# Kernel tuning notes

Measured on AMD Instinct MI355X. Metric: run time of the kernel, lower is better.

The kernel has to match this reference:

```python
import jax, jax.numpy as jnp
import numpy as np

DIM = 1024
NUM_HEADS = 16
HEAD_DIM = DIM // NUM_HEADS


def setup_inputs() -> dict:
    key = jax.random.key(0)
    k1, k2, k3, k4 = jax.random.split(key, 4)
    x = jax.random.normal(k1, (4, 4096, DIM), dtype=jnp.float32)
    # nn.Linear(dim, 3*dim, bias=False): weight [3*dim, dim]
    w_qkv = jax.random.normal(k2, (3 * DIM, DIM), dtype=jnp.float32) * (1.0 / np.sqrt(DIM))
    # nn.Linear(dim, dim): weight [dim, dim], bias [dim]
    w_proj = jax.random.normal(k3, (DIM, DIM), dtype=jnp.float32) * (1.0 / np.sqrt(DIM))
    b_proj = jax.random.normal(k4, (DIM,), dtype=jnp.float32) * 0.01
    return {"x": x, "w_qkv": w_qkv, "w_proj": w_proj, "b_proj": b_proj}


def reference(x, w_qkv, w_proj, b_proj):
    B, N, C = x.shape
    H, D = NUM_HEADS, C // NUM_HEADS
    # qkv projection: [B,N,3C] -> [3,B,H,N,D]
    qkv = (x @ w_qkv.T).reshape(B, N, 3, H, D).transpose(2, 0, 3, 1, 4)
    q, k, v = qkv[0], qkv[1], qkv[2]
    # elu(x)+1 feature map
    q = jax.nn.elu(q) + 1.0
    k = jax.nn.elu(k) + 1.0
    # kv outer-product aggregation: [B,H,D,D]
    kv = jnp.einsum('bhnd,bhne->bhde', k, v)
    # numerator: [B,H,N,D]
    num = jnp.einsum('bhnd,bhde->bhne', q, kv)
    # normalizer: [B,H,N]
    z = 1.0 / (jnp.einsum('bhnd,bhd->bhn', q, k.sum(axis=2)) + 1e-6)
    out = num * z[..., None]  # [B,H,N,D]
    out = out.transpose(0, 2, 1, 3).reshape(B, N, C)
    return out @ w_proj.T + b_proj
```

## Files before the change

kernel.cpp:

```cpp
#include <hip/hip_runtime.h>
#include <hip/hip_bf16.h>
#include <stdint.h>


typedef unsigned short u16;
typedef __attribute__((ext_vector_type(4))) float f32x4;
typedef __attribute__((ext_vector_type(8))) __bf16 bf16x8;
typedef __attribute__((ext_vector_type(4))) unsigned short us4;
typedef __attribute__((ext_vector_type(8))) unsigned short us8;

typedef __attribute__((address_space(3))) unsigned as3u;
typedef const __attribute__((address_space(1))) unsigned as1u;

__device__ __forceinline__ float bf2f(u16 u) {
  union { unsigned i; float f; } x; x.i = ((unsigned)u) << 16; return x.f;
}
__device__ __forceinline__ u16 f2bf(float f) {
  union { float f; unsigned i; } x; x.f = f;
  return (u16)((x.i + 0x7FFFu + ((x.i >> 16) & 1u)) >> 16);
}
__device__ __forceinline__ void gload16(const u16* g, u16* l) {
  __builtin_amdgcn_global_load_lds((as1u*)g, (as3u*)l, 16, 0, 0);
}
__device__ __forceinline__ bf16x8 ld8(const u16* p) { return *(const bf16x8*)p; }

#define BAR asm volatile("s_barrier" ::: "memory")
#define VMC4 asm volatile("s_waitcnt vmcnt(4)" ::: "memory")
#define VMC0 asm volatile("s_waitcnt vmcnt(0)" ::: "memory")

#define CVT_O1 4194304
#define CVT_O2 4980736
#define CVT_O3 5242880
__global__ __launch_bounds__(256) void cvt_all(
    const float* __restrict__ x, const float* __restrict__ wqkv,
    const float* __restrict__ wproj, u16* __restrict__ xb,
    u16* __restrict__ wqkvb, u16* __restrict__ wprojb) {
  int i = blockIdx.x * 256 + threadIdx.x;
  const float* src;
  u16* dst;
  int off;
  if (i < CVT_O1) { src = x; dst = xb; off = i; }
  else if (i < CVT_O2) { src = wqkv; dst = wqkvb; off = i - CVT_O1; }
  else if (i < CVT_O3) { src = wproj; dst = wprojb; off = i - CVT_O2; }
  else return;
  f32x4 v = ((const f32x4*)src)[off];
  us4 o;
  o[0] = f2bf(v[0]); o[1] = f2bf(v[1]); o[2] = f2bf(v[2]); o[3] = f2bf(v[3]);
  ((us4*)dst)[off] = o;
}

template <int EPI>
__device__ __forceinline__ void gemm256_body(
    const u16* __restrict__ A, const u16* __restrict__ B, int Ncols,
    u16* __restrict__ oQ, u16* __restrict__ oKT, u16* __restrict__ oVT,
    const float* __restrict__ bias, float* __restrict__ oF, u16* ldsb) {
  constexpr int K = 1024;
  constexpr int NITER = 8;

  const int bid = blockIdx.x;
  const int tm = (bid & 7) * 8 + ((bid >> 3) & 7);
  const int tn = bid >> 6;
  const int m0 = tm << 8, n0 = tn << 8;
  const int t = threadIdx.x;
  const int w = t >> 6, lane = t & 63;
  const int wm = w >> 2, wn = w & 3;
  const int l15 = lane & 15, l4 = lane >> 4;

  const u16* Ab = A + (size_t)m0 * K;
  const u16* Bb = B + (size_t)n0 * K;

  int srcoff[2][2];
  #pragma unroll
  for (int l = 0; l < 2; ++l) {
    int c = l * 512 + t;
    int row = c >> 3, ch = c & 7;
    #pragma unroll
    for (int h = 0; h < 2; ++h) {
      int rr = row + h * 128;
      srcoff[l][h] = rr * K + (ch ^ (rr & 7)) * 8;
    }
  }

#define LDSAT(buf, mat) (ldsb + ((buf) * 2 + (mat)) * (256 * 64))

#define STAGE(mat, buf, h, kt)                                                \
  {                                                                           \
    const u16* gsrc = ((mat) ? Bb : Ab) + (kt) * 64;                          \
    _Pragma("unroll") for (int l = 0; l < 2; ++l)                             \
        gload16(gsrc + srcoff[l][h],                                          \
                LDSAT(buf, mat) + (l * 512 + w * 64) * 8 + (h) * 128 * 64);   \
  }

#define LDA(buf, q)                                                           \
  _Pragma("unroll") for (int i = 0; i < 2; ++i)                               \
  _Pragma("unroll") for (int kk = 0; kk < 2; ++kk) {                          \
    int row = wm * 128 + (q) * 32 + i * 16 + l15;                             \
    int ch = (kk * 4 + l4) ^ (row & 7);                                       \
    a[i][kk] = ld8(LDSAT(buf, 0) + row * 64 + ch * 8);                        \
  }

#define LDB(buf)                                                              \
  _Pragma("unroll") for (int j = 0; j < 4; ++j)                               \
  _Pragma("unroll") for (int kk = 0; kk < 2; ++kk) {                          \
    int row = wn * 64 + j * 16 + l15;                                         \
    int ch = (kk * 4 + l4) ^ (row & 7);                                       \
    b[j][kk] = ld8(LDSAT(buf, 1) + row * 64 + ch * 8);                        \
  }

#define MFMA16(q)                                                             \
  __builtin_amdgcn_s_setprio(1);                                              \
  _Pragma("unroll") for (int i = 0; i < 2; ++i)                               \
  _Pragma("unroll") for (int kk = 0; kk < 2; ++kk)                            \
  _Pragma("unroll") for (int j = 0; j < 4; ++j)                               \
    acc[(q) * 2 + i][j] = __builtin_amdgcn_mfma_f32_16x16x32_bf16(            \
        a[i][kk], b[j][kk], acc[(q) * 2 + i][j], 0, 0, 0);                    \
  __builtin_amdgcn_s_setprio(0);

  f32x4 acc[8][4] = {};
  bf16x8 a[2][2], b[4][2];

  STAGE(1, 0, 0, 0); STAGE(1, 0, 1, 0);
  STAGE(0, 0, 0, 0); STAGE(0, 0, 1, 0);
  STAGE(1, 1, 0, 1); STAGE(1, 1, 1, 1);
  VMC4;
  BAR;

  for (int J = 0; J < NITER; ++J) {
    const int t2 = 2 * J + 2, t3 = 2 * J + 3;
    const bool more = (J < NITER - 1);
    LDB(0); LDA(0, 0);
    STAGE(0, 1, 0, 2 * J + 1);
    BAR; MFMA16(0); BAR;
    LDA(0, 1);
    STAGE(0, 1, 1, 2 * J + 1);
    BAR; MFMA16(1); BAR;
    LDA(0, 2);
    if (more) STAGE(1, 0, 0, t2);
    BAR; MFMA16(2); BAR;
    LDA(0, 3);
    if (more) STAGE(1, 0, 1, t2);
    BAR; MFMA16(3);
    if (more) { VMC4; } else { VMC0; }
    BAR;
    LDB(1); LDA(1, 0);
    if (more) STAGE(0, 0, 0, t2);
    BAR; MFMA16(0); BAR;
    LDA(1, 1);
    if (more) STAGE(0, 0, 1, t2);
    BAR; MFMA16(1); BAR;
    LDA(1, 2);
    if (more) STAGE(1, 1, 0, t3);
    BAR; MFMA16(2); BAR;
    LDA(1, 3);
    if (more) STAGE(1, 1, 1, t3);
    BAR; MFMA16(3);
    if (more) { VMC4; } else { VMC0; }
    BAR;
  }

  if constexpr (EPI == 0) {
    const int part = n0 >> 10;
    if (part == 0) {
      u16* sb = ldsb;
      __syncthreads();
      #pragma unroll
      for (int fi = 0; fi < 8; ++fi) {
        #pragma unroll
        for (int j = 0; j < 4; ++j) {
          #pragma unroll
          for (int rr = 0; rr < 4; ++rr) {
            int m = wm * 128 + fi * 16 + l4 * 4 + rr;
            int c = wn * 64 + j * 16 + l15;
            float val = acc[fi][j][rr];
            val = val > 0.f ? val + 1.f : __expf(val);
            sb[m * 256 + (c ^ (((m >> 2) & 3) << 4))] = f2bf(val);
          }
        }
      }
      __syncthreads();
      #pragma unroll
      for (int i = 0; i < 16; ++i) {
        int idx = i * 512 + t;
        int rr = idx >> 5, g = idx & 31;
        int gs = g ^ (((rr >> 2) & 3) << 1);
        us8 vv = *(const us8*)&sb[rr * 256 + gs * 8];
        int n = (m0 + rr) & 4095, bb = (m0 + rr) >> 12;
        int c = n0 + g * 8;
        int h = c >> 6, d = c & 63;
        *(us8*)&oQ[(((size_t)(bb * 16 + h)) * 4096 + n) * 64 + d] = vv;
      }
    } else {
      #pragma unroll
      for (int j = 0; j < 4; ++j) {
        const int col = n0 + wn * 64 + j * 16 + l15;
        const int cc = col & 1023;
        const int h = cc >> 6, d = cc & 63;
        #pragma unroll
        for (int fi = 0; fi < 8; ++fi) {
          const int mbase = m0 + wm * 128 + fi * 16 + l4 * 4;
          const int bb = mbase >> 12, n = mbase & 4095;
          const int bh = bb * 16 + h;
          us4 o;
          #pragma unroll
          for (int rr = 0; rr < 4; ++rr) {
            float val = acc[fi][j][rr];
            if (part == 1) val = val > 0.f ? val + 1.f : __expf(val);
            o[rr] = f2bf(val);
          }
          u16* dst = (part == 1) ? oKT : oVT;
          *(us4*)&dst[(((size_t)bh) * 64 + d) * 4096 + n] = o;
        }
      }
    }
  } else {
    #pragma unroll
    for (int fi = 0; fi < 8; ++fi) {
      const int mbase = m0 + wm * 128 + fi * 16 + l4 * 4;
      #pragma unroll
      for (int j = 0; j < 4; ++j) {
        const int col = n0 + wn * 64 + j * 16 + l15;
        #pragma unroll
        for (int rr = 0; rr < 4; ++rr)
          oF[(size_t)(mbase + rr) * 1024 + col] = acc[fi][j][rr] + bias[col];
      }
    }
  }
#undef STAGE
#undef LDA
#undef LDB
#undef MFMA16
#undef LDSAT
}

__global__ __launch_bounds__(512) void gemm_qkv(
    const u16* __restrict__ A, const u16* __restrict__ B,
    u16* __restrict__ oQ, u16* __restrict__ oKT, u16* __restrict__ oVT) {
  __shared__ u16 lds[2 * 2 * 256 * 64];
  gemm256_body<0>(A, B, 3072, oQ, oKT, oVT, nullptr, nullptr, lds);
}

__global__ __launch_bounds__(512) void gemm_proj(
    const u16* __restrict__ A, const u16* __restrict__ B,
    const float* __restrict__ bias, float* __restrict__ oF) {
  __shared__ u16 lds[2 * 2 * 256 * 64];
  gemm256_body<1>(A, B, 1024, nullptr, nullptr, nullptr, bias, oF, lds);
}

__global__ __launch_bounds__(256) void kv_mfma(const u16* __restrict__ kTg,
                                               const u16* __restrict__ vTg,
                                               float* __restrict__ kv_part,
                                               float* __restrict__ ksum_part) {
  __shared__ u16 kTl[64 * 256];
  __shared__ u16 vTl[64 * 256];
  const int blk = blockIdx.x;
  const int bh = blk >> 4, s = blk & 15;
  const int n0 = s * 256;
  const int t = threadIdx.x;
  const int w = t >> 6, lane = t & 63;
  const int wr = w >> 1, wc = w & 1;
  const int l15 = lane & 15, l4 = lane >> 4;

  const u16* kg = kTg + ((size_t)bh * 64) * 4096 + n0;
  const u16* vg = vTg + ((size_t)bh * 64) * 4096 + n0;
  #pragma unroll
  for (int i = 0; i < 8; ++i) {
    int c = i * 256 + t;
    int row = c >> 5, ch = c & 31;
    int sch = (ch & ~7) | ((ch ^ row) & 7);
    gload16(kg + (size_t)row * 4096 + sch * 8, &kTl[(i * 256 + w * 64) * 8]);
    gload16(vg + (size_t)row * 4096 + sch * 8, &vTl[(i * 256 + w * 64) * 8]);
  }
  __syncthreads();

  {
    const int row = t >> 2, q4 = t & 3;
    float sum = 0.f;
    #pragma unroll
    for (int j = 0; j < 8; ++j) {
      int p = q4 * 8 + ((j + row) & 7);
      us8 u = *(const us8*)&kTl[row * 256 + p * 8];
      #pragma unroll
      for (int x = 0; x < 8; ++x) sum += bf2f(u[x]);
    }
    sum += __shfl_xor(sum, 1);
    sum += __shfl_xor(sum, 2);
    if ((t & 3) == 0) ksum_part[((size_t)s * 64 + bh) * 64 + row] = sum;
  }

  f32x4 acc[2][2] = {};
  #pragma unroll
  for (int kk = 0; kk < 8; ++kk) {
    bf16x8 a[2], b[2];
    #pragma unroll
    for (int i = 0; i < 2; ++i) {
      int row = wr * 32 + i * 16 + l15;
      int p = (kk * 4 + l4) ^ (row & 7);
      a[i] = ld8(&kTl[row * 256 + p * 8]);
    }
    #pragma unroll
    for (int j = 0; j < 2; ++j) {
      int row = wc * 32 + j * 16 + l15;
      int p = (kk * 4 + l4) ^ (row & 7);
      b[j] = ld8(&vTl[row * 256 + p * 8]);
    }
    #pragma unroll
    for (int i = 0; i < 2; ++i)
      #pragma unroll
      for (int j = 0; j < 2; ++j)
        acc[i][j] = __builtin_amdgcn_mfma_f32_16x16x32_bf16(a[i], b[j], acc[i][j], 0, 0, 0);
  }
  float* dst = kv_part + ((size_t)s * 64 + bh) * 4096;
  #pragma unroll
  for (int i = 0; i < 2; ++i)
    #pragma unroll
    for (int j = 0; j < 2; ++j)
      #pragma unroll
      for (int rr = 0; rr < 4; ++rr) {
        int d = wr * 32 + i * 16 + l4 * 4 + rr;
        int e = wc * 32 + j * 16 + l15;
        dst[e * 64 + d] = acc[i][j][rr];
      }
}

__global__ __launch_bounds__(256) void cvt_kv(const float* __restrict__ kv_part,
                                              const float* __restrict__ ksum_part,
                                              u16* __restrict__ kvTb) {
  const int blk = blockIdx.x;
  const int bh = blk >> 2, qtr = blk & 3;
  const int t = threadIdx.x;
  #pragma unroll
  for (int i = 0; i < 5; ++i) {
    int idx = qtr * 1280 + i * 256 + t;
    int row = idx >> 6, d = idx & 63;
    float s = 0.f;
    if (row < 64) {
      #pragma unroll
      for (int p = 0; p < 16; ++p)
        s += kv_part[((size_t)p * 64 + bh) * 4096 + idx];
    } else if (row == 64) {
      #pragma unroll
      for (int p = 0; p < 16; ++p)
        s += ksum_part[((size_t)p * 64 + bh) * 64 + d];
    }
    kvTb[(size_t)bh * 5120 + idx] = f2bf(s);
  }
}

__global__ __launch_bounds__(256) void numz_mfma(const u16* __restrict__ qg,
                                                 const u16* __restrict__ kvTb,
                                                 u16* __restrict__ attn) {
  __shared__ u16 ql[128 * 64];
  __shared__ u16 bl[80 * 64];
  const int blk = blockIdx.x;
  const int bh = blk >> 5, c5 = blk & 31;
  const int t = threadIdx.x;
  const int w = t >> 6, lane = t & 63;
  const int l15 = lane & 15, l4 = lane >> 4;
  const int bb = bh >> 4, h = bh & 15;

  const u16* qp = qg + ((size_t)bh * 4096 + c5 * 128) * 64;
  #pragma unroll
  for (int i = 0; i < 4; ++i) {
    int c = i * 256 + t;
    int row = c >> 3, ch = c & 7;
    gload16(qp + (size_t)row * 64 + ((ch ^ row) & 7) * 8, &ql[(i * 256 + w * 64) * 8]);
  }
  {
    const us4* bsrc = (const us4*)(kvTb + (size_t)bh * 5120);
    #pragma unroll
    for (int i = 0; i < 5; ++i) {
      int idx = i * 256 + t;
      int row = idx >> 4;
      ((us4*)bl)[idx ^ ((row & 7) << 1)] = bsrc[idx];
    }
  }
  __syncthreads();

  f32x4 acc[2][5] = {};
  #pragma unroll
  for (int kk = 0; kk < 2; ++kk) {
    bf16x8 a[2], b[5];
    #pragma unroll
    for (int i = 0; i < 2; ++i) {
      int row = w * 32 + i * 16 + l15;
      int p = (kk * 4 + l4) ^ (row & 7);
      a[i] = ld8(&ql[row * 64 + p * 8]);
    }
    #pragma unroll
    for (int j = 0; j < 5; ++j) {
      int row = j * 16 + l15;
      int p = (kk * 4 + l4) ^ (row & 7);
      b[j] = ld8(&bl[row * 64 + p * 8]);
    }
    #pragma unroll
    for (int i = 0; i < 2; ++i)
      #pragma unroll
      for (int j = 0; j < 5; ++j)
        acc[i][j] = __builtin_amdgcn_mfma_f32_16x16x32_bf16(a[i], b[j], acc[i][j], 0, 0, 0);
  }

  #pragma unroll
  for (int i = 0; i < 2; ++i)
    #pragma unroll
    for (int rr = 0; rr < 4; ++rr) {
      int m = w * 32 + i * 16 + l4 * 4 + rr;
      int n = c5 * 128 + m;
      float zv = __shfl(acc[i][4][rr], lane & 48);
      float zz = 1.f / (zv + 1e-6f);
      u16* op = attn + ((size_t)bb * 4096 + n) * 1024 + h * 64;
      #pragma unroll
      for (int j = 0; j < 4; ++j)
        op[j * 16 + l15] = f2bf(acc[i][j][rr] * zz);
    }
}

extern "C" void kernel_launch(void* const* d_in, const int* in_sizes, int n_in,
                              void* d_out, int out_size, void* d_ws, size_t ws_size,
                              hipStream_t stream) {
  const float* x = (const float*)d_in[0];
  const float* w_qkv = (const float*)d_in[1];
  const float* w_proj = (const float*)d_in[2];
  const float* b_proj = (const float*)d_in[3];
  float* out = (float*)d_out;
  char* ws = (char*)d_ws;

  u16* xb        = (u16*)(ws);
  float* kv_part = (float*)(ws);
  u16* attn      = (u16*)(ws);
  u16* wqkvb     = (u16*)(ws + 33554432);
  u16* wprojb    = (u16*)(ws + 39845888);
  u16* q         = (u16*)(ws + 41943040);
  u16* kT        = (u16*)(ws + 75497472);
  u16* vT        = (u16*)(ws + 109051904);
  float* ksum_p  = (float*)(ws + 142606336);
  u16* kvTb      = (u16*)(ws + 142868480);

  cvt_all<<<20480, 256, 0, stream>>>(x, w_qkv, w_proj, xb, wqkvb, wprojb);
  gemm_qkv<<<64 * 12, 512, 0, stream>>>(xb, wqkvb, q, kT, vT);
  kv_mfma<<<1024, 256, 0, stream>>>(kT, vT, kv_part, ksum_p);
  cvt_kv<<<256, 256, 0, stream>>>(kv_part, ksum_p, kvTb);
  numz_mfma<<<2048, 256, 0, stream>>>(q, kvTb, attn);
  gemm_proj<<<64 * 4, 512, 0, stream>>>(attn, wprojb, b_proj, out);
}
```

Before: 310.8 us.

## Switch GEMM inner loop to 32x32x16 MFMA and remap proj tile order

Replaces the 16x16x32 bf16 MFMA tiling with 32x32x16 MFMAs in the shared 256x256 GEMM body. This halves the LDS fragment loads per MFMA and uses the larger instruction, which has higher throughput per issue. The epilogues are rewritten for the 32x32 accumulator layout. The block-to-tile mapping for the projection GEMM is also changed to improve L2 reuse. The cost is a different register footprint and different LDS access patterns, which may cause bank conflicts with the existing swizzle.

```diff
diff --git a/kernel.cpp b/kernel.cpp
--- a/kernel.cpp
+++ b/kernel.cpp
@@ -5,6 +5,7 @@
 
 typedef unsigned short u16;
 typedef __attribute__((ext_vector_type(4))) float f32x4;
+typedef __attribute__((ext_vector_type(16))) float f32x16;
 typedef __attribute__((ext_vector_type(8))) __bf16 bf16x8;
 typedef __attribute__((ext_vector_type(4))) unsigned short us4;
 typedef __attribute__((ext_vector_type(8))) unsigned short us8;
@@ -58,13 +59,19 @@
   constexpr int NITER = 8;
 
   const int bid = blockIdx.x;
-  const int tm = (bid & 7) * 8 + ((bid >> 3) & 7);
-  const int tn = bid >> 6;
+  int tm, tn;
+  if constexpr (EPI == 1) {
+    tm = (bid & 7) * 8 + (bid >> 5);
+    tn = (bid >> 3) & 3;
+  } else {
+    tm = (bid & 7) * 8 + ((bid >> 3) & 7);
+    tn = bid >> 6;
+  }
   const int m0 = tm << 8, n0 = tn << 8;
   const int t = threadIdx.x;
   const int w = t >> 6, lane = t & 63;
   const int wm = w >> 2, wn = w & 3;
-  const int l15 = lane & 15, l4 = lane >> 4;
+  const int l31 = lane & 31, lhi = lane >> 5;
 
   const u16* Ab = A + (size_t)m0 * K;
   const u16* Bb = B + (size_t)n0 * K;
@@ -91,33 +98,31 @@
                 LDSAT(buf, mat) + (l * 512 + w * 64) * 8 + (h) * 128 * 64);   \
   }
 
-#define LDA(buf, q)                                                           \
-  _Pragma("unroll") for (int i = 0; i < 2; ++i)                               \
-  _Pragma("unroll") for (int kk = 0; kk < 2; ++kk) {                          \
-    int row = wm * 128 + (q) * 32 + i * 16 + l15;                             \
-    int ch = (kk * 4 + l4) ^ (row & 7);                                       \
-    a[i][kk] = ld8(LDSAT(buf, 0) + row * 64 + ch * 8);                        \
+#define LDA(buf, mi)                                                          \
+  _Pragma("unroll") for (int kk = 0; kk < 4; ++kk) {                          \
+    int row = wm * 128 + (mi) * 32 + l31;                                     \
+    int ch = (kk * 2 + lhi) ^ (row & 7);                                      \
+    a[kk] = ld8(LDSAT(buf, 0) + row * 64 + ch * 8);                           \
   }
 
 #define LDB(buf)                                                              \
-  _Pragma("unroll") for (int j = 0; j < 4; ++j)                               \
-  _Pragma("unroll") for (int kk = 0; kk < 2; ++kk) {                          \
-    int row = wn * 64 + j * 16 + l15;                                         \
-    int ch = (kk * 4 + l4) ^ (row & 7);                                       \
-    b[j][kk] = ld8(LDSAT(buf, 1) + row * 64 + ch * 8);                        \
-  }
-
-#define MFMA16(q)                                                             \
+  _Pragma("unroll") for (int nj = 0; nj < 2; ++nj)                            \
+  _Pragma("unroll") for (int kk = 0; kk < 4; ++kk) {                          \
+    int row = wn * 64 + nj * 32 + l31;                                        \
+    int ch = (kk * 2 + lhi) ^ (row & 7);                                      \
+    b[nj][kk] = ld8(LDSAT(buf, 1) + row * 64 + ch * 8);                       \
+  }
+
+#define MFMA8(mi)                                                             \
   __builtin_amdgcn_s_setprio(1);                                              \
-  _Pragma("unroll") for (int i = 0; i < 2; ++i)                               \
-  _Pragma("unroll") for (int kk = 0; kk < 2; ++kk)                            \
-  _Pragma("unroll") for (int j = 0; j < 4; ++j)                               \
-    acc[(q) * 2 + i][j] = __builtin_amdgcn_mfma_f32_16x16x32_bf16(            \
-        a[i][kk], b[j][kk], acc[(q) * 2 + i][j], 0, 0, 0);                    \
+  _Pragma("unroll") for (int kk = 0; kk < 4; ++kk)                            \
+  _Pragma("unroll") for (int nj = 0; nj < 2; ++nj)                            \
+    acc[mi][nj] = __builtin_amdgcn_mfma_f32_32x32x16_bf16(                    \
+        a[kk], b[nj][kk], acc[mi][nj], 0, 0, 0);                              \
   __builtin_amdgcn_s_setprio(0);
 
-  f32x4 acc[8][4] = {};
-  bf16x8 a[2][2], b[4][2];
+  f32x16 acc[4][2] = {};
+  bf16x8 a[4], b[2][4];
 
   STAGE(1, 0, 0, 0); STAGE(1, 0, 1, 0);
   STAGE(0, 0, 0, 0); STAGE(0, 0, 1, 0);
@@ -130,30 +135,30 @@
     const bool more = (J < NITER - 1);
     LDB(0); LDA(0, 0);
     STAGE(0, 1, 0, 2 * J + 1);
-    BAR; MFMA16(0); BAR;
+    BAR; MFMA8(0); BAR;
     LDA(0, 1);
     STAGE(0, 1, 1, 2 * J + 1);
-    BAR; MFMA16(1); BAR;
+    BAR; MFMA8(1); BAR;
     LDA(0, 2);
     if (more) STAGE(1, 0, 0, t2);
-    BAR; MFMA16(2); BAR;
+    BAR; MFMA8(2); BAR;
     LDA(0, 3);
     if (more) STAGE(1, 0, 1, t2);
-    BAR; MFMA16(3);
+    BAR; MFMA8(3);
     if (more) { VMC4; } else { VMC0; }
     BAR;
     LDB(1); LDA(1, 0);
     if (more) STAGE(0, 0, 0, t2);
-    BAR; MFMA16(0); BAR;
+    BAR; MFMA8(0); BAR;
     LDA(1, 1);
     if (more) STAGE(0, 0, 1, t2);
-    BAR; MFMA16(1); BAR;
+    BAR; MFMA8(1); BAR;
     LDA(1, 2);
     if (more) STAGE(1, 1, 0, t3);
-    BAR; MFMA16(2); BAR;
+    BAR; MFMA8(2); BAR;
     LDA(1, 3);
     if (more) STAGE(1, 1, 1, t3);
-    BAR; MFMA16(3);
+    BAR; MFMA8(3);
     if (more) { VMC4; } else { VMC0; }
     BAR;
   }
@@ -164,14 +169,14 @@
       u16* sb = ldsb;
       __syncthreads();
       #pragma unroll
-      for (int fi = 0; fi < 8; ++fi) {
+      for (int mi = 0; mi < 4; ++mi) {
         #pragma unroll
-        for (int j = 0; j < 4; ++j) {
+        for (int nj = 0; nj < 2; ++nj) {
           #pragma unroll
-          for (int rr = 0; rr < 4; ++rr) {
-            int m = wm * 128 + fi * 16 + l4 * 4 + rr;
-            int c = wn * 64 + j * 16 + l15;
-            float val = acc[fi][j][rr];
+          for (int r = 0; r < 16; ++r) {
+            int m = wm * 128 + mi * 32 + 4 * lhi + (r & 3) + 8 * (r >> 2);
+            int c = wn * 64 + nj * 32 + l31;
+            float val = acc[mi][nj][r];
             val = val > 0.f ? val + 1.f : __expf(val);
             sb[m * 256 + (c ^ (((m >> 2) & 3) << 4))] = f2bf(val);
           }
@@ -191,44 +196,50 @@
       }
     } else {
       #pragma unroll
-      for (int j = 0; j < 4; ++j) {
-        const int col = n0 + wn * 64 + j * 16 + l15;
+      for (int nj = 0; nj < 2; ++nj) {
+        const int col = n0 + wn * 64 + nj * 32 + l31;
         const int cc = col & 1023;
         const int h = cc >> 6, d = cc & 63;
         #pragma unroll
-        for (int fi = 0; fi < 8; ++fi) {
-          const int mbase = m0 + wm * 128 + fi * 16 + l4 * 4;
-          const int bb = mbase >> 12, n = mbase & 4095;
-          const int bh = bb * 16 + h;
-          us4 o;
+        for (int mi = 0; mi < 4; ++mi) {
           #pragma unroll
-          for (int rr = 0; rr < 4; ++rr) {
-            float val = acc[fi][j][rr];
-            if (part == 1) val = val > 0.f ? val + 1.f : __expf(val);
-            o[rr] = f2bf(val);
+          for (int rg = 0; rg < 4; ++rg) {
+            const int mrow = m0 + wm * 128 + mi * 32 + 4 * lhi + 8 * rg;
+            const int bb = mrow >> 12, n = mrow & 4095;
+            const int bh = bb * 16 + h;
+            us4 o;
+            #pragma unroll
+            for (int rr = 0; rr < 4; ++rr) {
+              float val = acc[mi][nj][rg * 4 + rr];
+              if (part == 1) val = val > 0.f ? val + 1.f : __expf(val);
+              o[rr] = f2bf(val);
+            }
+            u16* dst = (part == 1) ? oKT : oVT;
+            *(us4*)&dst[(((size_t)bh) * 64 + d) * 4096 + n] = o;
           }
-          u16* dst = (part == 1) ? oKT : oVT;
-          *(us4*)&dst[(((size_t)bh) * 64 + d) * 4096 + n] = o;
         }
       }
     }
   } else {
     #pragma unroll
-    for (int fi = 0; fi < 8; ++fi) {
-      const int mbase = m0 + wm * 128 + fi * 16 + l4 * 4;
-      #pragma unroll
-      for (int j = 0; j < 4; ++j) {
-        const int col = n0 + wn * 64 + j * 16 + l15;
+    for (int mi = 0; mi < 4; ++mi) {
+      #pragma unroll
+      for (int nj = 0; nj < 2; ++nj) {
+        const int col = n0 + wn * 64 + nj * 32 + l31;
         #pragma unroll
-        for (int rr = 0; rr < 4; ++rr)
-          oF[(size_t)(mbase + rr) * 1024 + col] = acc[fi][j][rr] + bias[col];
+        for (int rg = 0; rg < 4; ++rg) {
+          const int mrow = m0 + wm * 128 + mi * 32 + 4 * lhi + 8 * rg;
+          #pragma unroll
+          for (int rr = 0; rr < 4; ++rr)
+            oF[(size_t)(mrow + rr) * 1024 + col] = acc[mi][nj][rg * 4 + rr] + bias[col];
+        }
       }
     }
   }
 #undef STAGE
 #undef LDA
 #undef LDB
-#undef MFMA16
+#undef MFMA8
 #undef LDSAT
 }
 
```

Result: slower. 334.2 us (+7.5%).

## Fuse kv reduction into kv_mfma via last-block atomic, halve numz grid

Applied to the files above, without the earlier changes.

Removes the separate cvt_kv launch. The last of the 16 kv_mfma blocks for each head, found with an atomic counter, now sums the partials and writes the bf16 kv/ksum tile. numz_mfma blocks each handle two 128-row chunks so the kv tile is loaded into LDS once per two chunks. The gemm_proj tile mapping is also reordered for better L2 reuse of A/B tiles. The trade-offs are an extra memset, a serialized tail reduction done by a single block per head, and less parallelism in numz.

```diff
diff --git a/kernel.cpp b/kernel.cpp
--- a/kernel.cpp
+++ b/kernel.cpp
@@ -58,8 +58,14 @@
   constexpr int NITER = 8;
 
   const int bid = blockIdx.x;
-  const int tm = (bid & 7) * 8 + ((bid >> 3) & 7);
-  const int tn = bid >> 6;
+  int tm, tn;
+  if constexpr (EPI == 1) {
+    tm = (bid & 7) * 8 + (bid >> 5);
+    tn = (bid >> 3) & 3;
+  } else {
+    tm = (bid & 7) * 8 + ((bid >> 3) & 7);
+    tn = bid >> 6;
+  }
   const int m0 = tm << 8, n0 = tn << 8;
   const int t = threadIdx.x;
   const int w = t >> 6, lane = t & 63;
@@ -249,9 +255,12 @@
 __global__ __launch_bounds__(256) void kv_mfma(const u16* __restrict__ kTg,
                                                const u16* __restrict__ vTg,
                                                float* __restrict__ kv_part,
-                                               float* __restrict__ ksum_part) {
+                                               float* __restrict__ ksum_part,
+                                               u16* __restrict__ kvTb,
+                                               unsigned* __restrict__ cnt) {
   __shared__ u16 kTl[64 * 256];
   __shared__ u16 vTl[64 * 256];
+  __shared__ unsigned lastdone;
   const int blk = blockIdx.x;
   const int bh = blk >> 4, s = blk & 15;
   const int n0 = s * 256;
@@ -320,29 +329,31 @@
         int e = wc * 32 + j * 16 + l15;
         dst[e * 64 + d] = acc[i][j][rr];
       }
-}
-
-__global__ __launch_bounds__(256) void cvt_kv(const float* __restrict__ kv_part,
-                                              const float* __restrict__ ksum_part,
-                                              u16* __restrict__ kvTb) {
-  const int blk = blockIdx.x;
-  const int bh = blk >> 2, qtr = blk & 3;
-  const int t = threadIdx.x;
-  #pragma unroll
-  for (int i = 0; i < 5; ++i) {
-    int idx = qtr * 1280 + i * 256 + t;
-    int row = idx >> 6, d = idx & 63;
-    float s = 0.f;
-    if (row < 64) {
-      #pragma unroll
-      for (int p = 0; p < 16; ++p)
-        s += kv_part[((size_t)p * 64 + bh) * 4096 + idx];
-    } else if (row == 64) {
-      #pragma unroll
-      for (int p = 0; p < 16; ++p)
-        s += ksum_part[((size_t)p * 64 + bh) * 64 + d];
-    }
-    kvTb[(size_t)bh * 5120 + idx] = f2bf(s);
+
+  __syncthreads();
+  if (t == 0) {
+    __threadfence();
+    lastdone = (atomicAdd(&cnt[bh], 1u) == 15u) ? 1u : 0u;
+  }
+  __syncthreads();
+  if (lastdone) {
+    __threadfence();
+    #pragma unroll
+    for (int i = 0; i < 20; ++i) {
+      int idx = i * 256 + t;
+      int row = idx >> 6, d = idx & 63;
+      float s2 = 0.f;
+      if (row < 64) {
+        #pragma unroll
+        for (int p = 0; p < 16; ++p)
+          s2 += kv_part[((size_t)p * 64 + bh) * 4096 + idx];
+      } else if (row == 64) {
+        #pragma unroll
+        for (int p = 0; p < 16; ++p)
+          s2 += ksum_part[((size_t)p * 64 + bh) * 64 + d];
+      }
+      kvTb[(size_t)bh * 5120 + idx] = f2bf(s2);
+    }
   }
 }
 
@@ -352,19 +363,12 @@
   __shared__ u16 ql[128 * 64];
   __shared__ u16 bl[80 * 64];
   const int blk = blockIdx.x;
-  const int bh = blk >> 5, c5 = blk & 31;
+  const int bh = blk >> 4, cbase = (blk & 15) * 2;
   const int t = threadIdx.x;
   const int w = t >> 6, lane = t & 63;
   const int l15 = lane & 15, l4 = lane >> 4;
   const int bb = bh >> 4, h = bh & 15;
 
-  const u16* qp = qg + ((size_t)bh * 4096 + c5 * 128) * 64;
-  #pragma unroll
-  for (int i = 0; i < 4; ++i) {
-    int c = i * 256 + t;
-    int row = c >> 3, ch = c & 7;
-    gload16(qp + (size_t)row * 64 + ((ch ^ row) & 7) * 8, &ql[(i * 256 + w * 64) * 8]);
-  }
   {
     const us4* bsrc = (const us4*)(kvTb + (size_t)bh * 5120);
     #pragma unroll
@@ -374,44 +378,56 @@
       ((us4*)bl)[idx ^ ((row & 7) << 1)] = bsrc[idx];
     }
   }
-  __syncthreads();
-
-  f32x4 acc[2][5] = {};
-  #pragma unroll
-  for (int kk = 0; kk < 2; ++kk) {
-    bf16x8 a[2], b[5];
-    #pragma unroll
-    for (int i = 0; i < 2; ++i) {
-      int row = w * 32 + i * 16 + l15;
-      int p = (kk * 4 + l4) ^ (row & 7);
-      a[i] = ld8(&ql[row * 64 + p * 8]);
-    }
-    #pragma unroll
-    for (int j = 0; j < 5; ++j) {
-      int row = j * 16 + l15;
-      int p = (kk * 4 + l4) ^ (row & 7);
-      b[j] = ld8(&bl[row * 64 + p * 8]);
-    }
+
+  for (int cc = 0; cc < 2; ++cc) {
+    const int c5 = cbase + cc;
+    const u16* qp = qg + ((size_t)bh * 4096 + c5 * 128) * 64;
+    #pragma unroll
+    for (int i = 0; i < 4; ++i) {
+      int c = i * 256 + t;
+      int row = c >> 3, ch = c & 7;
+      gload16(qp + (size_t)row * 64 + ((ch ^ row) & 7) * 8, &ql[(i * 256 + w * 64) * 8]);
+    }
+    __syncthreads();
+
+    f32x4 acc[2][5] = {};
+    #pragma unroll
+    for (int kk = 0; kk < 2; ++kk) {
+      bf16x8 a[2], b[5];
+      #pragma unroll
+      for (int i = 0; i < 2; ++i) {
+        int row = w * 32 + i * 16 + l15;
+        int p = (kk * 4 + l4) ^ (row & 7);
+        a[i] = ld8(&ql[row * 64 + p * 8]);
+      }
+      #pragma unroll
+      for (int j = 0; j < 5; ++j) {
+        int row = j * 16 + l15;
+        int p = (kk * 4 + l4) ^ (row & 7);
+        b[j] = ld8(&bl[row * 64 + p * 8]);
+      }
+      #pragma unroll
+      for (int i = 0; i < 2; ++i)
+        #pragma unroll
+        for (int j = 0; j < 5; ++j)
+          acc[i][j] = __builtin_amdgcn_mfma_f32_16x16x32_bf16(a[i], b[j], acc[i][j], 0, 0, 0);
+    }
+
     #pragma unroll
     for (int i = 0; i < 2; ++i)
       #pragma unroll
-      for (int j = 0; j < 5; ++j)
-        acc[i][j] = __builtin_amdgcn_mfma_f32_16x16x32_bf16(a[i], b[j], acc[i][j], 0, 0, 0);
-  }
-
-  #pragma unroll
-  for (int i = 0; i < 2; ++i)
-    #pragma unroll
-    for (int rr = 0; rr < 4; ++rr) {
-      int m = w * 32 + i * 16 + l4 * 4 + rr;
-      int n = c5 * 128 + m;
-      float zv = __shfl(acc[i][4][rr], lane & 48);
-      float zz = 1.f / (zv + 1e-6f);
-      u16* op = attn + ((size_t)bb * 4096 + n) * 1024 + h * 64;
-      #pragma unroll
-      for (int j = 0; j < 4; ++j)
-        op[j * 16 + l15] = f2bf(acc[i][j][rr] * zz);
-    }
+      for (int rr = 0; rr < 4; ++rr) {
+        int m = w * 32 + i * 16 + l4 * 4 + rr;
+        int n = c5 * 128 + m;
+        float zv = __shfl(acc[i][4][rr], lane & 48);
+        float zz = 1.f / (zv + 1e-6f);
+        u16* op = attn + ((size_t)bb * 4096 + n) * 1024 + h * 64;
+        #pragma unroll
+        for (int j = 0; j < 4; ++j)
+          op[j * 16 + l15] = f2bf(acc[i][j][rr] * zz);
+      }
+    if (cc == 0) __syncthreads();
+  }
 }
 
 extern "C" void kernel_launch(void* const* d_in, const int* in_sizes, int n_in,
@@ -434,11 +450,12 @@
   u16* vT        = (u16*)(ws + 109051904);
   float* ksum_p  = (float*)(ws + 142606336);
   u16* kvTb      = (u16*)(ws + 142868480);
-
+  unsigned* cnt  = (unsigned*)(ws + 143523840);
+
+  hipMemsetAsync(cnt, 0, 256, stream);
   cvt_all<<<20480, 256, 0, stream>>>(x, w_qkv, w_proj, xb, wqkvb, wprojb);
   gemm_qkv<<<64 * 12, 512, 0, stream>>>(xb, wqkvb, q, kT, vT);
-  kv_mfma<<<1024, 256, 0, stream>>>(kT, vT, kv_part, ksum_p);
-  cvt_kv<<<256, 256, 0, stream>>>(kv_part, ksum_p, kvTb);
-  numz_mfma<<<2048, 256, 0, stream>>>(q, kvTb, attn);
+  kv_mfma<<<1024, 256, 0, stream>>>(kT, vT, kv_part, ksum_p, kvTb, cnt);
+  numz_mfma<<<1024, 256, 0, stream>>>(q, kvTb, attn);
   gemm_proj<<<64 * 4, 512, 0, stream>>>(attn, wprojb, b_proj, out);
 }
```

Result: slower. 399.8 us (+28.6%).
